# Performance work log

Hardware: AMD Instinct MI355X
Metric: run time of the kernel (lower is better)

Reference implementation:

```python
import jax, jax.numpy as jnp
import numpy as np

B, S, F = 4, 2048, 8
D, H, L, FF = 256, 8, 2, 1024
DH = D // H
NSK, NPAT = 2000, 64
DQ = D // 4  # pattern/feat sub-embedding width


def setup_inputs() -> dict:
    key = jax.random.key(0)
    ks = jax.random.split(key, 32)
    r = lambda i, shape: jax.random.normal(ks[i], shape, jnp.float32) * 0.02
    return {
        'interactions': jax.random.randint(ks[0], (B, S), 0, 2 * NSK),
        'patterns': jax.random.randint(ks[1], (B, S), 0, NPAT),
        'forget_features': jax.random.normal(ks[2], (B, S, F), jnp.float32),
        'inter_emb': r(3, (2 * NSK, D)),
        'pattern_emb': r(4, (NPAT, DQ)),
        'feat_W': r(5, (F, DQ)), 'feat_b': jnp.zeros((DQ,), jnp.float32),
        'in_W': r(6, (D + 2 * DQ, D)), 'in_b': jnp.zeros((D,), jnp.float32),
        'time_W': r(7, (1, D)), 'time_b': jnp.zeros((D,), jnp.float32),
        'pos_W': r(8, (1, D)), 'pos_b': jnp.zeros((D,), jnp.float32),
        'Wq': r(9, (L, D, H, DH)), 'bq': jnp.zeros((L, H, DH), jnp.float32),
        'Wk': r(10, (L, D, H, DH)), 'bk': jnp.zeros((L, H, DH), jnp.float32),
        'Wv': r(11, (L, D, H, DH)), 'bv': jnp.zeros((L, H, DH), jnp.float32),
        'Wo': r(12, (L, H, DH, D)), 'bo': jnp.zeros((L, D), jnp.float32),
        'kerple_p': jnp.full((L, H, 1, 1), 0.5, jnp.float32),
        'kerple_a': jnp.zeros((L, H, 1, 1), jnp.float32),
        'ln1_g': jnp.ones((L, D), jnp.float32), 'ln1_b': jnp.zeros((L, D), jnp.float32),
        'ln2_g': jnp.ones((L, D), jnp.float32), 'ln2_b': jnp.zeros((L, D), jnp.float32),
        'ffn_W1': r(13, (L, D, FF)), 'ffn_b1': jnp.zeros((L, FF), jnp.float32),
        'ffn_W2': r(14, (L, FF, D)), 'ffn_b2': jnp.zeros((L, D), jnp.float32),
        'out_W': r(15, (D, NSK)), 'out_b': jnp.zeros((NSK,), jnp.float32),
    }


def _ln(x, g, b, eps=1e-6):
    m = jnp.mean(x, -1, keepdims=True)
    v = jnp.mean(jnp.square(x - m), -1, keepdims=True)
    return g * (x - m) * jax.lax.rsqrt(v + eps) + b


def reference(interactions, patterns, forget_features, inter_emb, pattern_emb,
              feat_W, feat_b, in_W, in_b, time_W, time_b, pos_W, pos_b,
              Wq, bq, Wk, bk, Wv, bv, Wo, bo, kerple_p, kerple_a,
              ln1_g, ln1_b, ln2_g, ln2_b, ffn_W1, ffn_b1, ffn_W2, ffn_b2,
              out_W, out_b):
    inter_e = inter_emb[interactions]                      # [B,S,D]
    pat_e = pattern_emb[patterns]                          # [B,S,D/4]
    feat_e = forget_features @ feat_W + feat_b             # [B,S,D/4]
    x = jnp.concatenate([inter_e, pat_e, feat_e], -1) @ in_W + in_b  # [B,S,D]
    elapsed = forget_features[:, :, 0:1]
    time_enc = jnp.tanh(elapsed @ time_W + time_b)
    pos = jnp.arange(S, dtype=jnp.float32)[None, :, None] / jnp.float32(S)
    pos_enc = pos @ pos_W + pos_b
    x = x + time_enc + pos_enc

    positions = jnp.arange(S, dtype=jnp.float32)
    dist = jnp.maximum(positions[:, None] - positions[None, :], 0.0)  # [S,S]
    causal_bias = jnp.triu(jnp.full((S, S), -1e9, jnp.float32), 1)    # [S,S]
    inv_sqrt_dh = 1.0 / jnp.sqrt(jnp.float32(DH))

    for i in range(L):
        p = jax.nn.softplus(kerple_p[i])                   # [H,1,1]
        a = jax.nn.softplus(kerple_a[i])
        bias = causal_bias[None] - p * jnp.log1p(a * dist[None])  # [H,S,S]
        q = jnp.einsum('bsd,dhk->bshk', x, Wq[i]) + bq[i]
        k = jnp.einsum('bsd,dhk->bshk', x, Wk[i]) + bk[i]
        v = jnp.einsum('bsd,dhk->bshk', x, Wv[i]) + bv[i]
        scores = jnp.einsum('bshk,bthk->bhst', q, k) * inv_sqrt_dh + bias[None]
        attn = jax.nn.softmax(scores, axis=-1)
        o = jnp.einsum('bhst,bthk->bshk', attn, v)
        attn_out = jnp.einsum('bshk,hkd->bsd', o, Wo[i]) + bo[i]
        x = _ln(x + attn_out, ln1_g[i], ln1_b[i])
        h = jax.nn.gelu(x @ ffn_W1[i] + ffn_b1[i], approximate=False)
        ffn_out = h @ ffn_W2[i] + ffn_b2[i]
        x = _ln(x + ffn_out, ln2_g[i], ln2_b[i])
    return x @ out_W + out_b
```

## Files before the change

### kernel.cpp

```cpp
#include <hip/hip_runtime.h>
#include <math.h>

#define SEQ   2048
#define BATCH 4
#define NTOK  8192
#define DM    256
#define NHD   8
#define DHD   32
#define DFF   1024
#define NSKC  2000

typedef __attribute__((ext_vector_type(8))) short short8;
typedef __attribute__((ext_vector_type(4))) float f32x4;
typedef unsigned short ushort_t;

#define QPRE ((float)(0.17677669529663687 * 1.4426950408889634))

__device__ __forceinline__ ushort_t f2bf(float x) {
    union { float f; unsigned u; } c; c.f = x;
    unsigned r = c.u + 0x7FFFu + ((c.u >> 16) & 1u);
    return (ushort_t)(r >> 16);
}

#if __has_builtin(__builtin_amdgcn_cvt_pk_bf16_f32)
typedef __attribute__((ext_vector_type(2))) __bf16 bf16x2_t;
__device__ __forceinline__ unsigned pack_bf16(float a, float b) {
    bf16x2_t r = __builtin_amdgcn_cvt_pk_bf16_f32(a, b);
    union { bf16x2_t v; unsigned u; } c; c.v = r;
    return c.u;
}
#else
__device__ __forceinline__ unsigned pack_bf16(float a, float b) {
    return (unsigned)f2bf(a) | ((unsigned)f2bf(b) << 16);
}
#endif

__device__ __forceinline__ float bf2f(ushort_t x) {
    union { unsigned u; float f; } c; c.u = ((unsigned)x) << 16;
    return c.f;
}

struct ConvSeg { const float* src; ushort_t* dst; int K; int N; int ntx; int base; };
struct ConvArgs { ConvSeg s[14]; };

__global__ __launch_bounds__(256) void convert_kernel(ConvArgs args) {
    int bid = blockIdx.x;
    int si = 0;
#pragma unroll
    for (int i = 1; i < 14; i++) if (bid >= args.s[i].base) si = i;
    ConvSeg sg = args.s[si];
    int local = bid - sg.base;
    int ty = local / sg.ntx;
    int tx = local - ty * sg.ntx;
    int n0 = tx * 32, k0 = ty * 32;
    __shared__ float T[32][33];
    int tid = threadIdx.x;
    int tn = tid & 31, tk4 = tid >> 5;
#pragma unroll
    for (int i = 0; i < 4; i++) {
        int kl = tk4 + i * 8;
        float v = 0.0f;
        if (n0 + tn < sg.N) v = sg.src[(size_t)(k0 + kl) * sg.N + n0 + tn];
        T[kl][tn] = v;
    }
    __syncthreads();
    int tk = tid & 31, tn4 = tid >> 5;
#pragma unroll
    for (int i = 0; i < 4; i++) {
        int nl = tn4 + i * 8;
        sg.dst[(size_t)(n0 + nl) * sg.K + k0 + tk] = f2bf(T[tk][nl]);
    }
}

__global__ __launch_bounds__(384) void concat_kernel(
    const int* __restrict__ interactions, const int* __restrict__ patterns,
    const float* __restrict__ ff, const float* __restrict__ inter_emb,
    const float* __restrict__ pattern_emb, const float* __restrict__ feat_W,
    const float* __restrict__ feat_b, ushort_t* __restrict__ out)
{
    int tok = blockIdx.x;
    int j = threadIdx.x;
    float v;
    if (j < 256) {
        v = inter_emb[(size_t)interactions[tok] * 256 + j];
    } else if (j < 320) {
        v = pattern_emb[patterns[tok] * 64 + (j - 256)];
    } else {
        int c = j - 320;
        float acc = feat_b[c];
#pragma unroll
        for (int f = 0; f < 8; f++) acc += ff[tok * 8 + f] * feat_W[f * 64 + c];
        v = acc;
    }
    out[(size_t)tok * 384 + j] = f2bf(v);
}

__global__ __launch_bounds__(256) void ln_kernel(
    float* __restrict__ x, const ushort_t* __restrict__ r,
    const float* __restrict__ g, const float* __restrict__ b,
    ushort_t* __restrict__ xb)
{
    int tok = blockIdx.x;
    int d = threadIdx.x;
    size_t idx = (size_t)tok * DM + d;
    float v = x[idx] + bf2f(r[idx]);
    float s1 = v, s2 = v * v;
#pragma unroll
    for (int off = 32; off > 0; off >>= 1) {
        s1 += __shfl_down(s1, off, 64);
        s2 += __shfl_down(s2, off, 64);
    }
    __shared__ float red1[4], red2[4];
    int wid = d >> 6, lane = d & 63;
    if (lane == 0) { red1[wid] = s1; red2[wid] = s2; }
    __syncthreads();
    s1 = red1[0] + red1[1] + red1[2] + red1[3];
    s2 = red2[0] + red2[1] + red2[2] + red2[3];
    float mean = s1 * (1.0f / 256.0f);
    float var = s2 * (1.0f / 256.0f) - mean * mean;
    float inv = rsqrtf(var + 1e-6f);
    float nv = g[d] * (v - mean) * inv + b[d];
    x[idx] = nv;
    xb[idx] = f2bf(nv);
}

__global__ __launch_bounds__(256) void gemm64(
    const ushort_t* __restrict__ A, const ushort_t* __restrict__ Bt,
    int M, int N, int K, int mode,
    float* __restrict__ Cf, ushort_t* __restrict__ Cb,
    const float* __restrict__ b0,
    const float* __restrict__ ffg, const float* __restrict__ tW,
    const float* __restrict__ tb, const float* __restrict__ pW,
    const float* __restrict__ pb)
{
    __shared__ ushort_t As[64][40];
    __shared__ ushort_t Bs[64][40];
    int m0 = blockIdx.y * 64, n0 = blockIdx.x * 64;
    int tid = threadIdx.x;
    int wv = tid >> 6, lane = tid & 63;
    int quad = lane >> 4, l16 = lane & 15;
    int srow = tid >> 2, sc = (tid & 3) << 3;

    f32x4 acc[4];
#pragma unroll
    for (int j = 0; j < 4; j++) acc[j] = (f32x4){0.f, 0.f, 0.f, 0.f};

    uint4 pa = *(const uint4*)&A[(size_t)(m0 + srow) * K + sc];
    uint4 pbv = *(const uint4*)&Bt[(size_t)(n0 + srow) * K + sc];

    int mrow = wv * 16;
    for (int k0 = 0; k0 < K; k0 += 32) {
        __syncthreads();
        *(uint4*)&As[srow][sc] = pa;
        *(uint4*)&Bs[srow][sc] = pbv;
        __syncthreads();
        if (k0 + 32 < K) {
            pa = *(const uint4*)&A[(size_t)(m0 + srow) * K + k0 + 32 + sc];
            pbv = *(const uint4*)&Bt[(size_t)(n0 + srow) * K + k0 + 32 + sc];
        }
        short8 af = *(const short8*)&As[mrow + l16][quad * 8];
        short8 bf0 = *(const short8*)&Bs[l16][quad * 8];
        short8 bf1 = *(const short8*)&Bs[16 + l16][quad * 8];
        short8 bf2 = *(const short8*)&Bs[32 + l16][quad * 8];
        short8 bf3 = *(const short8*)&Bs[48 + l16][quad * 8];
        acc[0] = __builtin_amdgcn_mfma_f32_16x16x32_bf16(af, bf0, acc[0], 0, 0, 0);
        acc[1] = __builtin_amdgcn_mfma_f32_16x16x32_bf16(af, bf1, acc[1], 0, 0, 0);
        acc[2] = __builtin_amdgcn_mfma_f32_16x16x32_bf16(af, bf2, acc[2], 0, 0, 0);
        acc[3] = __builtin_amdgcn_mfma_f32_16x16x32_bf16(af, bf3, acc[3], 0, 0, 0);
    }

#pragma unroll
    for (int r = 0; r < 4; r++) {
        int m = m0 + mrow + quad * 4 + r;
        if (mode == 4) {
            int s = m & (SEQ - 1);
            float el = ffg[m * 8];
            float pos = (float)s * (1.0f / (float)SEQ);
#pragma unroll
            for (int nt = 0; nt < 4; nt++) {
                int n = n0 + nt * 16 + l16;
                float te = tanhf(el * tW[n] + tb[n]);
                float pe = pos * pW[n] + pb[n];
                float nv = acc[nt][r] + b0[n] + te + pe;
                Cf[(size_t)m * N + n] = nv;
                Cb[(size_t)m * N + n] = f2bf(nv);
            }
        } else {
#pragma unroll
            for (int nt = 0; nt < 4; nt++) {
                int n = n0 + nt * 16 + l16;
                Cb[(size_t)m * N + n] = f2bf(acc[nt][r] + b0[n]);
            }
        }
    }
}

__global__ __launch_bounds__(256) void gemm_bf16_128(
    const ushort_t* __restrict__ A, const ushort_t* __restrict__ Bt,
    int M, int N, int K, int mode,
    float* __restrict__ Cf, ushort_t* __restrict__ Cb,
    ushort_t* __restrict__ Ck, ushort_t* __restrict__ Cv,
    const float* __restrict__ b0, const float* __restrict__ b1,
    const float* __restrict__ b2, int Nreal)
{
    __shared__ ushort_t As[128][40];
    __shared__ ushort_t Bs[128][40];
    int m0 = blockIdx.y * 128, n0 = blockIdx.x * 128;
    int tid = threadIdx.x;
    int wv = tid >> 6, lane = tid & 63;
    int quad = lane >> 4, l16 = lane & 15;
    int wm = (wv >> 1) * 64, wn = (wv & 1) * 64;
    int srow = tid >> 1, sc = (tid & 1) << 4;

    f32x4 acc[4][4];
#pragma unroll
    for (int i = 0; i < 4; i++)
#pragma unroll
        for (int j = 0; j < 4; j++) acc[i][j] = (f32x4){0.f, 0.f, 0.f, 0.f};

    uint4 pa0 = *(const uint4*)&A[(size_t)(m0 + srow) * K + sc];
    uint4 pa1 = *(const uint4*)&A[(size_t)(m0 + srow) * K + sc + 8];
    uint4 pb0 = *(const uint4*)&Bt[(size_t)(n0 + srow) * K + sc];
    uint4 pb1 = *(const uint4*)&Bt[(size_t)(n0 + srow) * K + sc + 8];

    for (int k0 = 0; k0 < K; k0 += 32) {
        __syncthreads();
        *(uint4*)&As[srow][sc] = pa0;
        *(uint4*)&As[srow][sc + 8] = pa1;
        *(uint4*)&Bs[srow][sc] = pb0;
        *(uint4*)&Bs[srow][sc + 8] = pb1;
        __syncthreads();
        if (k0 + 32 < K) {
            pa0 = *(const uint4*)&A[(size_t)(m0 + srow) * K + k0 + 32 + sc];
            pa1 = *(const uint4*)&A[(size_t)(m0 + srow) * K + k0 + 32 + sc + 8];
            pb0 = *(const uint4*)&Bt[(size_t)(n0 + srow) * K + k0 + 32 + sc];
            pb1 = *(const uint4*)&Bt[(size_t)(n0 + srow) * K + k0 + 32 + sc + 8];
        }
        short8 af[4], bf[4];
#pragma unroll
        for (int i = 0; i < 4; i++) {
            af[i] = *(const short8*)&As[wm + i * 16 + l16][quad * 8];
            bf[i] = *(const short8*)&Bs[wn + i * 16 + l16][quad * 8];
        }
#pragma unroll
        for (int i = 0; i < 4; i++)
#pragma unroll
            for (int j = 0; j < 4; j++)
                acc[i][j] = __builtin_amdgcn_mfma_f32_16x16x32_bf16(af[i], bf[j], acc[i][j], 0, 0, 0);
    }

#pragma unroll
    for (int i = 0; i < 4; i++) {
#pragma unroll
        for (int j = 0; j < 4; j++) {
            int n = n0 + wn + j * 16 + l16;
#pragma unroll
            for (int r = 0; r < 4; r++) {
                int m = m0 + wm + i * 16 + quad * 4 + r;
                float v = acc[i][j][r];
                if (mode == 1) {
                    float t = v + b0[n];
                    t = 0.5f * t * (1.0f + erff(t * 0.70710678118654752f));
                    Cb[(size_t)m * N + n] = f2bf(t);
                } else if (mode == 3) {
                    if (n < Nreal) Cf[(size_t)m * Nreal + n] = v + b0[n];
                } else {
                    int which = n >> 8, idx = n & 255;
                    int hh = idx >> 5, d = idx & 31;
                    int s = m & (SEQ - 1), b = m >> 11;
                    if (which == 0)
                        Cb[(((size_t)(b * NHD + hh)) * SEQ + s) * DHD + d] =
                            f2bf((v + b0[idx]) * QPRE);
                    else if (which == 1)
                        Ck[(((size_t)(b * NHD + hh)) * SEQ + s) * DHD + d] = f2bf(v + b1[idx]);
                    else {
                        int sp = (s & ~31) | (((s & 15) << 1) | ((s >> 4) & 1));
                        Cv[(((size_t)(b * NHD + hh)) * DHD + d) * SEQ + sp] = f2bf(v + b2[idx]);
                    }
                }
            }
        }
    }
}

__global__ __launch_bounds__(256) void attn_mfma(
    const ushort_t* __restrict__ qb, const ushort_t* __restrict__ kb,
    const ushort_t* __restrict__ vtb, const float* __restrict__ kp,
    const float* __restrict__ ka, ushort_t* __restrict__ ob)
{
    int h = blockIdx.y, b = blockIdx.z;
    int tid = threadIdx.x, wv = tid >> 6, lane = tid & 63;
    int quad = lane >> 4, l16 = lane & 15;
    int pair = wv >> 1, parity = wv & 1;

    __shared__ float tabs[2112];
    __shared__ ushort_t P2[4][2][16 * 40];
    __shared__ float Cmb[2][64][28];

    float p = log1pf(__expf(kp[h]));
    float a = log1pf(__expf(ka[h]));
    for (int i = tid; i < 2112; i += 256) {
        float w = 0.0f;
        if (i >= 64) w = exp2f(-p * __log2f(fmaf(a, (float)(i - 64), 1.0f)));
        tabs[i] = w;
    }
    __syncthreads();

    int bh = b * NHD + h;
    const ushort_t* Qh = qb + (size_t)bh * SEQ * DHD;
    const ushort_t* Kh = kb + (size_t)bh * SEQ * DHD;
    const ushort_t* Vh = vtb + (size_t)bh * DHD * SEQ;

    int pj = blockIdx.x * 2 + pair;
    int tlo = pj, thi = 127 - pj;
    int qlo0 = tlo * 16, qhi0 = thi * 16;

    short8 qfl = *(const short8*)&Qh[(qlo0 + l16) * DHD + quad * 8];
    short8 qfh = *(const short8*)&Qh[(qhi0 + l16) * DHD + quad * 8];
    f32x4 ol0 = (f32x4){0.f,0.f,0.f,0.f}, ol1 = (f32x4){0.f,0.f,0.f,0.f};
    f32x4 oh0 = (f32x4){0.f,0.f,0.f,0.f}, oh1 = (f32x4){0.f,0.f,0.f,0.f};
    float lsl[4] = {0.f,0.f,0.f,0.f}, lsh[4] = {0.f,0.f,0.f,0.f};
    ushort_t* Pl = &P2[wv][0][0];
    ushort_t* Ph = &P2[wv][1][0];

    int nch_hi = (thi + 2) >> 1;
    int nch_lo = (tlo + 2) >> 1;
    int qsrh = qhi0 + quad * 4;
    int qsrl = qlo0 + quad * 4;

    for (int ch = parity; ch < nch_hi; ch += 2) {
        int k0 = ch * 32;
        short8 kf0 = *(const short8*)&Kh[(k0 + l16) * DHD + quad * 8];
        short8 kf1 = *(const short8*)&Kh[(k0 + 16 + l16) * DHD + quad * 8];
        short8 vf0 = *(const short8*)&Vh[l16 * SEQ + k0 + quad * 8];
        short8 vf1 = *(const short8*)&Vh[(16 + l16) * SEQ + k0 + quad * 8];
        f32x4 z = (f32x4){0.f,0.f,0.f,0.f};

        f32x4 s0 = __builtin_amdgcn_mfma_f32_16x16x32_bf16(qfh, kf0, z, 0, 0, 0);
        f32x4 s1 = __builtin_amdgcn_mfma_f32_16x16x32_bf16(qfh, kf1, z, 0, 0, 0);
        {
            const float* tp = &tabs[qsrh - k0 - l16 + 48];
#pragma unroll
            for (int r = 0; r < 4; r++) {
                float e0 = exp2f(s0[r]) * tp[16 + r];
                float e1 = exp2f(s1[r]) * tp[r];
                lsh[r] += e0 + e1;
                *(unsigned*)&Ph[(quad * 4 + r) * 40 + l16 * 2] = pack_bf16(e0, e1);
            }
        }
        bool do_lo = (ch < nch_lo);
        if (do_lo) {
            f32x4 t0 = __builtin_amdgcn_mfma_f32_16x16x32_bf16(qfl, kf0, z, 0, 0, 0);
            f32x4 t1 = __builtin_amdgcn_mfma_f32_16x16x32_bf16(qfl, kf1, z, 0, 0, 0);
            const float* tq = &tabs[qsrl - k0 - l16 + 48];
#pragma unroll
            for (int r = 0; r < 4; r++) {
                float e0 = exp2f(t0[r]) * tq[16 + r];
                float e1 = exp2f(t1[r]) * tq[r];
                lsl[r] += e0 + e1;
                *(unsigned*)&Pl[(quad * 4 + r) * 40 + l16 * 2] = pack_bf16(e0, e1);
            }
        }

        __builtin_amdgcn_wave_barrier();
        short8 pfh = *(const short8*)&Ph[l16 * 40 + quad * 8];
        oh0 = __builtin_amdgcn_mfma_f32_16x16x32_bf16(pfh, vf0, oh0, 0, 0, 0);
        oh1 = __builtin_amdgcn_mfma_f32_16x16x32_bf16(pfh, vf1, oh1, 0, 0, 0);
        if (do_lo) {
            short8 pfl = *(const short8*)&Pl[l16 * 40 + quad * 8];
            ol0 = __builtin_amdgcn_mfma_f32_16x16x32_bf16(pfl, vf0, ol0, 0, 0, 0);
            ol1 = __builtin_amdgcn_mfma_f32_16x16x32_bf16(pfl, vf1, ol1, 0, 0, 0);
        }
    }

    if (parity == 1) {
        float* cp = &Cmb[pair][lane][0];
        *(float4*)&cp[0]  = (float4){oh0[0], oh0[1], oh0[2], oh0[3]};
        *(float4*)&cp[4]  = (float4){oh1[0], oh1[1], oh1[2], oh1[3]};
        *(float4*)&cp[8]  = (float4){ol0[0], ol0[1], ol0[2], ol0[3]};
        *(float4*)&cp[12] = (float4){ol1[0], ol1[1], ol1[2], ol1[3]};
        *(float4*)&cp[16] = (float4){lsh[0], lsh[1], lsh[2], lsh[3]};
        *(float4*)&cp[20] = (float4){lsl[0], lsl[1], lsl[2], lsl[3]};
    }
    __syncthreads();
    if (parity == 0) {
        const float* cp = &Cmb[pair][lane][0];
#pragma unroll
        for (int i = 0; i < 4; i++) {
            oh0[i] += cp[i];      oh1[i] += cp[4 + i];
            ol0[i] += cp[8 + i];  ol1[i] += cp[12 + i];
            lsh[i] += cp[16 + i]; lsl[i] += cp[20 + i];
        }
#pragma unroll
        for (int r = 0; r < 4; r++) {
#pragma unroll
            for (int off = 1; off < 16; off <<= 1) {
                lsh[r] += __shfl_xor(lsh[r], off, 16);
                lsl[r] += __shfl_xor(lsl[r], off, 16);
            }
        }
#pragma unroll
        for (int r = 0; r < 4; r++) {
            float rh = 1.0f / lsh[r];
            float rl = 1.0f / lsl[r];
            size_t bh_ = ((size_t)(b * SEQ + qsrh + r)) * DM + h * DHD;
            size_t bl_ = ((size_t)(b * SEQ + qsrl + r)) * DM + h * DHD;
            ob[bh_ + l16]      = f2bf(oh0[r] * rh);
            ob[bh_ + 16 + l16] = f2bf(oh1[r] * rh);
            ob[bl_ + l16]      = f2bf(ol0[r] * rl);
            ob[bl_ + 16 + l16] = f2bf(ol1[r] * rl);
        }
    }
}

extern "C" void kernel_launch(void* const* d_in, const int* in_sizes, int n_in,
                              void* d_out, int out_size, void* d_ws, size_t ws_size,
                              hipStream_t stream) {
    const int*   interactions = (const int*)d_in[0];
    const int*   patterns     = (const int*)d_in[1];
    const float* ff           = (const float*)d_in[2];
    const float* inter_emb    = (const float*)d_in[3];
    const float* pattern_emb  = (const float*)d_in[4];
    const float* feat_W       = (const float*)d_in[5];
    const float* feat_b       = (const float*)d_in[6];
    const float* in_W         = (const float*)d_in[7];
    const float* in_b         = (const float*)d_in[8];
    const float* time_W       = (const float*)d_in[9];
    const float* time_b       = (const float*)d_in[10];
    const float* pos_W        = (const float*)d_in[11];
    const float* pos_b        = (const float*)d_in[12];
    const float* Wq           = (const float*)d_in[13];
    const float* bq           = (const float*)d_in[14];
    const float* Wk           = (const float*)d_in[15];
    const float* bk           = (const float*)d_in[16];
    const float* Wv           = (const float*)d_in[17];
    const float* bv           = (const float*)d_in[18];
    const float* Wo           = (const float*)d_in[19];
    const float* bo           = (const float*)d_in[20];
    const float* kerple_p     = (const float*)d_in[21];
    const float* kerple_a     = (const float*)d_in[22];
    const float* ln1_g        = (const float*)d_in[23];
    const float* ln1_b        = (const float*)d_in[24];
    const float* ln2_g        = (const float*)d_in[25];
    const float* ln2_b        = (const float*)d_in[26];
    const float* ffn_W1       = (const float*)d_in[27];
    const float* ffn_b1       = (const float*)d_in[28];
    const float* ffn_W2       = (const float*)d_in[29];
    const float* ffn_b2       = (const float*)d_in[30];
    const float* out_W        = (const float*)d_in[31];
    const float* out_b        = (const float*)d_in[32];
    float* out = (float*)d_out;

    char* wsb = (char*)d_ws;
    const size_t MB = 1024 * 1024;
    float*    x    = (float*)(wsb + 0);
    ushort_t* tmpb = (ushort_t*)(wsb + 8  * MB);
    ushort_t* xb   = (ushort_t*)(wsb + 16 * MB);
    ushort_t* qbuf = (ushort_t*)(wsb + 20 * MB);
    ushort_t* kbuf = (ushort_t*)(wsb + 24 * MB);
    ushort_t* vtbf = (ushort_t*)(wsb + 28 * MB);
    ushort_t* shrd = (ushort_t*)(wsb + 32 * MB);
    ushort_t* cbuf = shrd;
    ushort_t* o_bf = shrd;
    ushort_t* h_bf = shrd;
    char* wp = wsb + 48 * MB;
    ushort_t* inWt  = (ushort_t*)wp;  wp += 256  * 384 * 2;
    ushort_t* qkvWt = (ushort_t*)wp;  wp += 2 * 768 * 256 * 2;
    ushort_t* WoT   = (ushort_t*)wp;  wp += 2 * 256 * 256 * 2;
    ushort_t* W1T   = (ushort_t*)wp;  wp += 2 * 1024 * 256 * 2;
    ushort_t* W2T   = (ushort_t*)wp;  wp += 2 * 256 * 1024 * 2;
    ushort_t* outWt = (ushort_t*)wp;  wp += 2048 * 256 * 2;

    ConvArgs ca;
    int D2 = 256 * 256;
    int base = 0, ib = 0;
    auto addseg = [&](const float* src, ushort_t* dst, int K, int N, int Npad) {
        ca.s[ib].src = src; ca.s[ib].dst = dst; ca.s[ib].K = K; ca.s[ib].N = N;
        ca.s[ib].ntx = Npad / 32; ca.s[ib].base = base;
        base += (Npad / 32) * (K / 32); ib++;
    };
    addseg(in_W,            inWt,           384,  256,  256);
    addseg(Wq,              qkvWt,          256,  256,  256);
    addseg(Wk,              qkvWt + 1 * D2, 256,  256,  256);
    addseg(Wv,              qkvWt + 2 * D2, 256,  256,  256);
    addseg(Wq + D2,         qkvWt + 3 * D2, 256,  256,  256);
    addseg(Wk + D2,         qkvWt + 4 * D2, 256,  256,  256);
    addseg(Wv + D2,         qkvWt + 5 * D2, 256,  256,  256);
    addseg(Wo,              WoT,            256,  256,  256);
    addseg(Wo + D2,         WoT + D2,       256,  256,  256);
    addseg(ffn_W1,          W1T,            256,  1024, 1024);
    addseg(ffn_W1 + 4 * D2, W1T + 4 * D2,   256,  1024, 1024);
    addseg(ffn_W2,          W2T,            1024, 256,  256);
    addseg(ffn_W2 + 4 * D2, W2T + 4 * D2,   1024, 256,  256);
    addseg(out_W,           outWt,          256,  2000, 2048);
    convert_kernel<<<base, 256, 0, stream>>>(ca);

    concat_kernel<<<NTOK, 384, 0, stream>>>(interactions, patterns, ff,
                                            inter_emb, pattern_emb, feat_W, feat_b, cbuf);
    gemm64<<<dim3(4, 128), 256, 0, stream>>>(cbuf, inWt, NTOK, 256, 384, 4,
                                             x, xb, in_b, ff, time_W, time_b, pos_W, pos_b);

    for (int l = 0; l < 2; l++) {
        gemm_bf16_128<<<dim3(6, 64), 256, 0, stream>>>(
            xb, qkvWt + (size_t)l * 768 * 256, NTOK, 768, 256, 2,
            nullptr, qbuf, kbuf, vtbf,
            bq + l * 256, bk + l * 256, bv + l * 256, 0);
        attn_mfma<<<dim3(32, NHD, BATCH), 256, 0, stream>>>(
            qbuf, kbuf, vtbf, kerple_p + l * NHD, kerple_a + l * NHD, o_bf);
        gemm64<<<dim3(4, 128), 256, 0, stream>>>(
            o_bf, WoT + (size_t)l * D2, NTOK, 256, 256, 5,
            nullptr, tmpb, bo + l * 256, nullptr, nullptr, nullptr, nullptr, nullptr);
        ln_kernel<<<NTOK, 256, 0, stream>>>(x, tmpb, ln1_g + l * 256, ln1_b + l * 256, xb);
        gemm_bf16_128<<<dim3(8, 64), 256, 0, stream>>>(
            xb, W1T + (size_t)l * 4 * D2, NTOK, 1024, 256, 1,
            nullptr, h_bf, nullptr, nullptr, ffn_b1 + l * 1024, nullptr, nullptr, 0);
        gemm64<<<dim3(4, 128), 256, 0, stream>>>(
            h_bf, W2T + (size_t)l * 4 * D2, NTOK, 256, 1024, 5,
            nullptr, tmpb, ffn_b2 + l * 256, nullptr, nullptr, nullptr, nullptr, nullptr);
        ln_kernel<<<NTOK, 256, 0, stream>>>(x, tmpb, ln2_g + l * 256, ln2_b + l * 256, xb);
    }

    gemm_bf16_128<<<dim3(16, 64), 256, 0, stream>>>(
        xb, outWt, NTOK, 2048, 256, 3,
        out, nullptr, nullptr, nullptr, out_b, nullptr, nullptr, NSKC);
}
```

Before: 483.1 us.

## Permute bf16 activation column layout to enable packed paired stores in GEMM epilogues

```diff
diff --git a/kernel.cpp b/kernel.cpp
--- a/kernel.cpp
+++ b/kernel.cpp
@@ -16,6 +16,8 @@
 
 #define QPRE ((float)(0.17677669529663687 * 1.4426950408889634))
 
+#define SPERM(i) (((i) & ~31) | (((i) & 15) << 1) | (((i) >> 4) & 1))
+
 __device__ __forceinline__ ushort_t f2bf(float x) {
     union { float f; unsigned u; } c; c.f = x;
     unsigned r = c.u + 0x7FFFu + ((c.u >> 16) & 1u);
@@ -40,7 +42,7 @@
     return c.f;
 }
 
-struct ConvSeg { const float* src; ushort_t* dst; int K; int N; int ntx; int base; };
+struct ConvSeg { const float* src; ushort_t* dst; int K; int N; int ntx; int base; int kperm; };
 struct ConvArgs { ConvSeg s[14]; };
 
 __global__ __launch_bounds__(256) void convert_kernel(ConvArgs args) {
@@ -65,10 +67,11 @@
     }
     __syncthreads();
     int tk = tid & 31, tn4 = tid >> 5;
+    int tks = sg.kperm ? (((tk & 15) << 1) | ((tk >> 4) & 1)) : tk;
 #pragma unroll
     for (int i = 0; i < 4; i++) {
         int nl = tn4 + i * 8;
-        sg.dst[(size_t)(n0 + nl) * sg.K + k0 + tk] = f2bf(T[tk][nl]);
+        sg.dst[(size_t)(n0 + nl) * sg.K + k0 + tks] = f2bf(T[tk][nl]);
     }
 }
 
@@ -102,8 +105,9 @@
 {
     int tok = blockIdx.x;
     int d = threadIdx.x;
-    size_t idx = (size_t)tok * DM + d;
-    float v = x[idx] + bf2f(r[idx]);
+    int ds = SPERM(d);
+    size_t row = (size_t)tok * DM;
+    float v = x[row + d] + bf2f(r[row + ds]);
     float s1 = v, s2 = v * v;
 #pragma unroll
     for (int off = 32; off > 0; off >>= 1) {
@@ -120,8 +124,8 @@
     float var = s2 * (1.0f / 256.0f) - mean * mean;
     float inv = rsqrtf(var + 1e-6f);
     float nv = g[d] * (v - mean) * inv + b[d];
-    x[idx] = nv;
-    xb[idx] = f2bf(nv);
+    x[row + d] = nv;
+    xb[row + ds] = f2bf(nv);
 }
 
 __global__ __launch_bounds__(256) void gemm64(
@@ -135,7 +139,7 @@
 {
     __shared__ ushort_t As[64][40];
     __shared__ ushort_t Bs[64][40];
-    int m0 = blockIdx.y * 64, n0 = blockIdx.x * 64;
+    int m0 = blockIdx.x * 64, n0 = blockIdx.y * 64;
     int tid = threadIdx.x;
     int wv = tid >> 6, lane = tid & 63;
     int quad = lane >> 4, l16 = lane & 15;
@@ -177,19 +181,22 @@
             float el = ffg[m * 8];
             float pos = (float)s * (1.0f / (float)SEQ);
 #pragma unroll
-            for (int nt = 0; nt < 4; nt++) {
-                int n = n0 + nt * 16 + l16;
-                float te = tanhf(el * tW[n] + tb[n]);
-                float pe = pos * pW[n] + pb[n];
-                float nv = acc[nt][r] + b0[n] + te + pe;
-                Cf[(size_t)m * N + n] = nv;
-                Cb[(size_t)m * N + n] = f2bf(nv);
+            for (int nt = 0; nt < 4; nt += 2) {
+                int nlo = n0 + nt * 16 + l16;
+                int nhi = nlo + 16;
+                float v0 = acc[nt][r] + b0[nlo] + tanhf(el * tW[nlo] + tb[nlo]) + pos * pW[nlo] + pb[nlo];
+                float v1 = acc[nt + 1][r] + b0[nhi] + tanhf(el * tW[nhi] + tb[nhi]) + pos * pW[nhi] + pb[nhi];
+                Cf[(size_t)m * N + nlo] = v0;
+                Cf[(size_t)m * N + nhi] = v1;
+                *(unsigned*)&Cb[(size_t)m * N + n0 + nt * 16 + 2 * l16] = pack_bf16(v0, v1);
             }
         } else {
 #pragma unroll
-            for (int nt = 0; nt < 4; nt++) {
-                int n = n0 + nt * 16 + l16;
-                Cb[(size_t)m * N + n] = f2bf(acc[nt][r] + b0[n]);
+            for (int nt = 0; nt < 4; nt += 2) {
+                int nlo = n0 + nt * 16 + l16;
+                float v0 = acc[nt][r] + b0[nlo];
+                float v1 = acc[nt + 1][r] + b0[nlo + 16];
+                *(unsigned*)&Cb[(size_t)m * N + n0 + nt * 16 + 2 * l16] = pack_bf16(v0, v1);
             }
         }
     }
@@ -205,7 +212,7 @@
 {
     __shared__ ushort_t As[128][40];
     __shared__ ushort_t Bs[128][40];
-    int m0 = blockIdx.y * 128, n0 = blockIdx.x * 128;
+    int m0 = blockIdx.x * 128, n0 = blockIdx.y * 128;
     int tid = threadIdx.x;
     int wv = tid >> 6, lane = tid & 63;
     int quad = lane >> 4, l16 = lane & 15;
@@ -252,30 +259,38 @@
 #pragma unroll
     for (int i = 0; i < 4; i++) {
 #pragma unroll
-        for (int j = 0; j < 4; j++) {
-            int n = n0 + wn + j * 16 + l16;
+        for (int jp = 0; jp < 4; jp += 2) {
+            int nlo = n0 + wn + jp * 16 + l16;
 #pragma unroll
             for (int r = 0; r < 4; r++) {
                 int m = m0 + wm + i * 16 + quad * 4 + r;
-                float v = acc[i][j][r];
+                float vlo = acc[i][jp][r];
+                float vhi = acc[i][jp + 1][r];
                 if (mode == 1) {
-                    float t = v + b0[n];
-                    t = 0.5f * t * (1.0f + erff(t * 0.70710678118654752f));
-                    Cb[(size_t)m * N + n] = f2bf(t);
+                    float t0 = vlo + b0[nlo];
+                    float t1 = vhi + b0[nlo + 16];
+                    t0 = 0.5f * t0 * (1.0f + erff(t0 * 0.70710678118654752f));
+                    t1 = 0.5f * t1 * (1.0f + erff(t1 * 0.70710678118654752f));
+                    *(unsigned*)&Cb[(size_t)m * N + n0 + wn + jp * 16 + 2 * l16] = pack_bf16(t0, t1);
                 } else if (mode == 3) {
-                    if (n < Nreal) Cf[(size_t)m * Nreal + n] = v + b0[n];
+                    if (nlo < Nreal)      Cf[(size_t)m * Nreal + nlo] = vlo + b0[nlo];
+                    if (nlo + 16 < Nreal) Cf[(size_t)m * Nreal + nlo + 16] = vhi + b0[nlo + 16];
                 } else {
-                    int which = n >> 8, idx = n & 255;
+                    int which = nlo >> 8, idx = nlo & 255;
                     int hh = idx >> 5, d = idx & 31;
                     int s = m & (SEQ - 1), b = m >> 11;
-                    if (which == 0)
-                        Cb[(((size_t)(b * NHD + hh)) * SEQ + s) * DHD + d] =
-                            f2bf((v + b0[idx]) * QPRE);
-                    else if (which == 1)
-                        Ck[(((size_t)(b * NHD + hh)) * SEQ + s) * DHD + d] = f2bf(v + b1[idx]);
-                    else {
+                    if (which == 0) {
+                        float q0 = (vlo + b0[idx]) * QPRE;
+                        float q1 = (vhi + b0[idx + 16]) * QPRE;
+                        *(unsigned*)&Cb[(((size_t)(b * NHD + hh)) * SEQ + s) * DHD + 2 * d] = pack_bf16(q0, q1);
+                    } else if (which == 1) {
+                        float k0v = vlo + b1[idx];
+                        float k1v = vhi + b1[idx + 16];
+                        *(unsigned*)&Ck[(((size_t)(b * NHD + hh)) * SEQ + s) * DHD + 2 * d] = pack_bf16(k0v, k1v);
+                    } else {
                         int sp = (s & ~31) | (((s & 15) << 1) | ((s >> 4) & 1));
-                        Cv[(((size_t)(b * NHD + hh)) * DHD + d) * SEQ + sp] = f2bf(v + b2[idx]);
+                        Cv[(((size_t)(b * NHD + hh)) * DHD + d) * SEQ + sp] = f2bf(vlo + b2[idx]);
+                        Cv[(((size_t)(b * NHD + hh)) * DHD + d + 16) * SEQ + sp] = f2bf(vhi + b2[idx + 16]);
                     }
                 }
             }
@@ -405,10 +420,8 @@
             float rl = 1.0f / lsl[r];
             size_t bh_ = ((size_t)(b * SEQ + qsrh + r)) * DM + h * DHD;
             size_t bl_ = ((size_t)(b * SEQ + qsrl + r)) * DM + h * DHD;
-            ob[bh_ + l16]      = f2bf(oh0[r] * rh);
-            ob[bh_ + 16 + l16] = f2bf(oh1[r] * rh);
-            ob[bl_ + l16]      = f2bf(ol0[r] * rl);
-            ob[bl_ + 16 + l16] = f2bf(ol1[r] * rl);
+            *(unsigned*)&ob[bh_ + 2 * l16] = pack_bf16(oh0[r] * rh, oh1[r] * rh);
+            *(unsigned*)&ob[bl_ + 2 * l16] = pack_bf16(ol0[r] * rl, ol1[r] * rl);
         }
     }
 }
@@ -474,53 +487,53 @@
     ConvArgs ca;
     int D2 = 256 * 256;
     int base = 0, ib = 0;
-    auto addseg = [&](const float* src, ushort_t* dst, int K, int N, int Npad) {
+    auto addseg = [&](const float* src, ushort_t* dst, int K, int N, int Npad, int kp) {
         ca.s[ib].src = src; ca.s[ib].dst = dst; ca.s[ib].K = K; ca.s[ib].N = N;
-        ca.s[ib].ntx = Npad / 32; ca.s[ib].base = base;
+        ca.s[ib].ntx = Npad / 32; ca.s[ib].base = base; ca.s[ib].kperm = kp;
         base += (Npad / 32) * (K / 32); ib++;
     };
-    addseg(in_W,            inWt,           384,  256,  256);
-    addseg(Wq,              qkvWt,          256,  256,  256);
-    addseg(Wk,              qkvWt + 1 * D2, 256,  256,  256);
-    addseg(Wv,              qkvWt + 2 * D2, 256,  256,  256);
-    addseg(Wq + D2,         qkvWt + 3 * D2, 256,  256,  256);
-    addseg(Wk + D2,         qkvWt + 4 * D2, 256,  256,  256);
-    addseg(Wv + D2,         qkvWt + 5 * D2, 256,  256,  256);
-    addseg(Wo,              WoT,            256,  256,  256);
-    addseg(Wo + D2,         WoT + D2,       256,  256,  256);
-    addseg(ffn_W1,          W1T,            256,  1024, 1024);
-    addseg(ffn_W1 + 4 * D2, W1T + 4 * D2,   256,  1024, 1024);
-    addseg(ffn_W2,          W2T,            1024, 256,  256);
-    addseg(ffn_W2 + 4 * D2, W2T + 4 * D2,   1024, 256,  256);
-    addseg(out_W,           outWt,          256,  2000, 2048);
+    addseg(in_W,            inWt,           384,  256,  256,  0);
+    addseg(Wq,              qkvWt,          256,  256,  256,  1);
+    addseg(Wk,              qkvWt + 1 * D2, 256,  256,  256,  1);
+    addseg(Wv,              qkvWt + 2 * D2, 256,  256,  256,  1);
+    addseg(Wq + D2,         qkvWt + 3 * D2, 256,  256,  256,  1);
+    addseg(Wk + D2,         qkvWt + 4 * D2, 256,  256,  256,  1);
+    addseg(Wv + D2,         qkvWt + 5 * D2, 256,  256,  256,  1);
+    addseg(Wo,              WoT,            256,  256,  256,  1);
+    addseg(Wo + D2,         WoT + D2,       256,  256,  256,  1);
+    addseg(ffn_W1,          W1T,            256,  1024, 1024, 1);
+    addseg(ffn_W1 + 4 * D2, W1T + 4 * D2,   256,  1024, 1024, 1);
+    addseg(ffn_W2,          W2T,            1024, 256,  256,  1);
+    addseg(ffn_W2 + 4 * D2, W2T + 4 * D2,   1024, 256,  256,  1);
+    addseg(out_W,           outWt,          256,  2000, 2048, 1);
     convert_kernel<<<base, 256, 0, stream>>>(ca);
 
     concat_kernel<<<NTOK, 384, 0, stream>>>(interactions, patterns, ff,
                                             inter_emb, pattern_emb, feat_W, feat_b, cbuf);
-    gemm64<<<dim3(4, 128), 256, 0, stream>>>(cbuf, inWt, NTOK, 256, 384, 4,
+    gemm64<<<dim3(128, 4), 256, 0, stream>>>(cbuf, inWt, NTOK, 256, 384, 4,
                                              x, xb, in_b, ff, time_W, time_b, pos_W, pos_b);
 
     for (int l = 0; l < 2; l++) {
-        gemm_bf16_128<<<dim3(6, 64), 256, 0, stream>>>(
+        gemm_bf16_128<<<dim3(64, 6), 256, 0, stream>>>(
             xb, qkvWt + (size_t)l * 768 * 256, NTOK, 768, 256, 2,
             nullptr, qbuf, kbuf, vtbf,
             bq + l * 256, bk + l * 256, bv + l * 256, 0);
         attn_mfma<<<dim3(32, NHD, BATCH), 256, 0, stream>>>(
             qbuf, kbuf, vtbf, kerple_p + l * NHD, kerple_a + l * NHD, o_bf);
-        gemm64<<<dim3(4, 128), 256, 0, stream>>>(
+        gemm64<<<dim3(128, 4), 256, 0, stream>>>(
             o_bf, WoT + (size_t)l * D2, NTOK, 256, 256, 5,
             nullptr, tmpb, bo + l * 256, nullptr, nullptr, nullptr, nullptr, nullptr);
         ln_kernel<<<NTOK, 256, 0, stream>>>(x, tmpb, ln1_g + l * 256, ln1_b + l * 256, xb);
-        gemm_bf16_128<<<dim3(8, 64), 256, 0, stream>>>(
+        gemm_bf16_128<<<dim3(64, 8), 256, 0, stream>>>(
             xb, W1T + (size_t)l * 4 * D2, NTOK, 1024, 256, 1,
             nullptr, h_bf, nullptr, nullptr, ffn_b1 + l * 1024, nullptr, nullptr, 0);
-        gemm64<<<dim3(4, 128), 256, 0, stream>>>(
+        gemm64<<<dim3(128, 4), 256, 0, stream>>>(
             h_bf, W2T + (size_t)l * 4 * D2, NTOK, 256, 1024, 5,
             nullptr, tmpb, ffn_b2 + l * 256, nullptr, nullptr, nullptr, nullptr, nullptr);
         ln_kernel<<<NTOK, 256, 0, stream>>>(x, tmpb, ln2_g + l * 256, ln2_b + l * 256, xb);
     }
 
-    gemm_bf16_128<<<dim3(16, 64), 256, 0, stream>>>(
+    gemm_bf16_128<<<dim3(64, 16), 256, 0, stream>>>(
         xb, outWt, NTOK, 2048, 256, 3,
         out, nullptr, nullptr, nullptr, out_b, nullptr, nullptr, NSKC);
 }
```

Result: faster. 450.5 us (-6.8%).
